# Kernel tuning notes

Measured on AMD Instinct MI355X. Metric: run time of the kernel, lower is better.

## Reference

```python
import jax, jax.numpy as jnp
import numpy as np

NUM_ITERATIONS = 100
EPS = 1e-6
LIPSCHITZ_COEFF = 0.9


def _l2_normalize(x, axis=None, eps=1e-12):
    return x * jax.lax.rsqrt((x * x).sum(axis=axis, keepdims=True) + eps)


def setup_inputs() -> dict:
    key = jax.random.key(0)
    k1, k2, k3, k4 = jax.random.split(key, 4)
    B, D_in, D_out = 32768, 1024, 1024
    x = jax.random.normal(k1, (B, D_in), dtype=jnp.float32)
    # TruncatedNormal(stddev=1/sqrt(fan_in)) approximated by scaled normal
    w = jax.random.normal(k2, (D_in, D_out), dtype=jnp.float32) / np.sqrt(D_in)
    b = jax.random.normal(k3, (D_out,), dtype=jnp.float32)
    u0 = jax.random.normal(k4, (1, D_out), dtype=jnp.float32)
    return {"x": x, "w": w, "b": b, "u0": u0}


def reference(x, w, b, u0):
    d_in = w.shape[0]

    # 100-step power iteration: tight sequential dependency chain of GEMV pairs.
    def body(i, carry):
        u, _ = carry
        v = _l2_normalize(jnp.matmul(u, w.T), eps=EPS)   # [1, d_in]
        u = _l2_normalize(jnp.matmul(v, w), eps=EPS)     # [1, d_out]
        return (u, v)

    v_init = jnp.zeros((1, d_in), dtype=w.dtype)
    u, v = jax.lax.fori_loop(0, NUM_ITERATIONS, body, (u0, v_init))
    u = jax.lax.stop_gradient(u)
    v = jax.lax.stop_gradient(v)

    sigma = jnp.matmul(jnp.matmul(v, w), u.T)[0, 0]      # spectral norm estimate
    factor = jnp.maximum(1.0, sigma / LIPSCHITZ_COEFF)
    w_norm = w / factor

    out = jnp.dot(x, w_norm) + b
    return out
```

## Files before the change

kernel.cpp:

```cpp
#include <hip/hip_runtime.h>
#include <hip/hip_bf16.h>
#include <cstdint>
#include <cstddef>

#define DDIM 1024
#define BROWS 32768

typedef __attribute__((ext_vector_type(8))) short short8;
typedef __attribute__((ext_vector_type(4))) float floatx4;

__device__ __forceinline__ float bf2f(unsigned short u) {
  return __uint_as_float(((unsigned int)u) << 16);
}
__device__ __forceinline__ unsigned short f2bf(float f) {
  unsigned int u = __float_as_uint(f);
  u += 0x7FFFu + ((u >> 16) & 1u);
  return (unsigned short)(u >> 16);
}

__device__ __forceinline__ void load_lds16(const void* g, void* l) {
  __builtin_amdgcn_global_load_lds(
      (const __attribute__((address_space(1))) unsigned int*)g,
      (__attribute__((address_space(3))) unsigned int*)l,
      16, 0, 0);
}

__global__ void __launch_bounds__(512, 2)
big_gemm(const float* __restrict__ Af, const unsigned short* __restrict__ Bt,
         float* __restrict__ Outf, const float* __restrict__ inv_ptr,
         const float* __restrict__ bias)
{
  __shared__ unsigned short As[128 * 32];
  __shared__ unsigned short Bs[256 * 32];

  const int tid  = threadIdx.x;
  const int lane = tid & 63;
  const int wid  = tid >> 6;
  const int wr = wid >> 2, wc = wid & 3;
  const int g = lane >> 4, r = lane & 15;

  const int bm0 = (int)(blockIdx.x & 255) * 128;
  const int bn0 = (int)(blockIdx.x >> 8) * 256;

  const floatx4 zero4 = {0.f, 0.f, 0.f, 0.f};
  floatx4 acc[4][4];
#pragma unroll
  for (int m = 0; m < 4; ++m)
#pragma unroll
    for (int n = 0; n < 4; ++n) acc[m][n] = zero4;

  for (int kk = 0; kk < DDIM; kk += 32) {
    __syncthreads();
#pragma unroll
    for (int p = 0; p < 2; ++p) {
      const int o = p * 8192 + tid * 16;
      const int row = o >> 6;
      const int cole = (o & 63) >> 1;
      load_lds16(Bt + (size_t)(bn0 + row) * DDIM + kk + cole, (char*)Bs + o);
    }
    {
      const int o = tid * 16;
      const int row = o >> 6;
      const int cole = (o & 63) >> 1;
      const float4* s = (const float4*)(Af + (size_t)(bm0 + row) * DDIM + kk + cole);
      float4 x0 = s[0], x1 = s[1];
      short8 t;
      t[0] = (short)f2bf(x0.x); t[1] = (short)f2bf(x0.y);
      t[2] = (short)f2bf(x0.z); t[3] = (short)f2bf(x0.w);
      t[4] = (short)f2bf(x1.x); t[5] = (short)f2bf(x1.y);
      t[6] = (short)f2bf(x1.z); t[7] = (short)f2bf(x1.w);
      *(short8*)((char*)As + o) = t;
    }
    __syncthreads();

    short8 afr[4], bfr[4];
#pragma unroll
    for (int m = 0; m < 4; ++m)
      afr[m] = *(const short8*)((const char*)As + (wr * 64 + m * 16 + r) * 64 + g * 16);
#pragma unroll
    for (int n = 0; n < 4; ++n)
      bfr[n] = *(const short8*)((const char*)Bs + (wc * 64 + n * 16 + r) * 64 + g * 16);
#pragma unroll
    for (int m = 0; m < 4; ++m)
#pragma unroll
      for (int n = 0; n < 4; ++n)
        acc[m][n] = __builtin_amdgcn_mfma_f32_16x16x32_bf16(afr[m], bfr[n], acc[m][n], 0, 0, 0);
  }

  const float inv = *inv_ptr;
#pragma unroll
  for (int n = 0; n < 4; ++n) {
    const int ocol = bn0 + wc * 64 + n * 16 + r;
    const float bv = bias[ocol];
#pragma unroll
    for (int m = 0; m < 4; ++m) {
      const int orow0 = bm0 + wr * 64 + m * 16 + g * 4;
#pragma unroll
      for (int q = 0; q < 4; ++q) {
        Outf[(size_t)(orow0 + q) * DDIM + ocol] = acc[m][n][q] * inv + bv;
      }
    }
  }
}

__global__ void __launch_bounds__(256, 2)
sq_gemm(const unsigned short* __restrict__ A, const unsigned short* __restrict__ Bt,
        unsigned short* __restrict__ Out, const float* __restrict__ in_max,
        float* __restrict__ out_max)
{
  __shared__ __align__(16) unsigned short As[2][4096];
  __shared__ __align__(16) unsigned short Bs[2][4096];
  __shared__ float redw[4];

  const int tid  = threadIdx.x;
  const int lane = tid & 63;
  const int wid  = tid >> 6;
  const int wr = wid >> 1, wc = wid & 1;
  const int g = lane >> 4, r = lane & 15;

  const int bm0 = (int)(blockIdx.x >> 4) * 64;
  const int bn0 = (int)(blockIdx.x & 15) * 64;

  const int so    = tid * 16;
  const int srow0 = so >> 7;
  const int sc16  = (so >> 4) & 7;
  const int scs   = sc16 ^ (srow0 & 7);
  const unsigned short* aSrc0 = A  + (size_t)(bm0 + srow0) * DDIM + scs * 8;
  const unsigned short* aSrc1 = A  + (size_t)(bm0 + 32 + srow0) * DDIM + scs * 8;
  const unsigned short* bSrc0 = Bt + (size_t)(bn0 + srow0) * DDIM + scs * 8;
  const unsigned short* bSrc1 = Bt + (size_t)(bn0 + 32 + srow0) * DDIM + scs * 8;

  const floatx4 zero4 = {0.f, 0.f, 0.f, 0.f};
  floatx4 acc[2][2];
#pragma unroll
  for (int fm = 0; fm < 2; ++fm)
#pragma unroll
    for (int fn = 0; fn < 2; ++fn) acc[fm][fn] = zero4;

  load_lds16(aSrc0, (char*)&As[0][0] + so);
  load_lds16(aSrc1, (char*)&As[0][0] + 4096 + so);
  load_lds16(bSrc0, (char*)&Bs[0][0] + so);
  load_lds16(bSrc1, (char*)&Bs[0][0] + 4096 + so);
  __syncthreads();

  int buf = 0;
  for (int t = 0; t < 16; ++t) {
    if (t + 1 < 16) {
      const int kk = (t + 1) * 64;
      load_lds16(aSrc0 + kk, (char*)&As[buf ^ 1][0] + so);
      load_lds16(aSrc1 + kk, (char*)&As[buf ^ 1][0] + 4096 + so);
      load_lds16(bSrc0 + kk, (char*)&Bs[buf ^ 1][0] + so);
      load_lds16(bSrc1 + kk, (char*)&Bs[buf ^ 1][0] + 4096 + so);
    }
#pragma unroll
    for (int ks = 0; ks < 2; ++ks) {
      const int chunk = ((ks << 2) + g) ^ (r & 7);
      short8 af[2], bf[2];
#pragma unroll
      for (int fm = 0; fm < 2; ++fm) {
        const int arow = wr * 32 + fm * 16 + r;
        af[fm] = *(const short8*)((const char*)&As[buf][0] + (arow << 7) + (chunk << 4));
      }
#pragma unroll
      for (int fn = 0; fn < 2; ++fn) {
        const int brow = wc * 32 + fn * 16 + r;
        bf[fn] = *(const short8*)((const char*)&Bs[buf][0] + (brow << 7) + (chunk << 4));
      }
#pragma unroll
      for (int fm = 0; fm < 2; ++fm)
#pragma unroll
        for (int fn = 0; fn < 2; ++fn)
          acc[fm][fn] = __builtin_amdgcn_mfma_f32_16x16x32_bf16(af[fm], bf[fn], acc[fm][fn], 0, 0, 0);
    }
    __syncthreads();
    buf ^= 1;
  }

  float c = 1.0f;
  if (in_max != nullptr) {
    int e;
    (void)frexpf(*in_max, &e);
    c = ldexpf(1.0f, -e);
  }
  const float c2 = c * c;
  float lmax = 0.0f;
#pragma unroll
  for (int fm = 0; fm < 2; ++fm) {
#pragma unroll
    for (int fn = 0; fn < 2; ++fn) {
      const int ocol = bn0 + wc * 32 + fn * 16 + r;
#pragma unroll
      for (int q = 0; q < 4; ++q) {
        const int orow = bm0 + wr * 32 + fm * 16 + g * 4 + q;
        float v = acc[fm][fn][q] * c2;
        Out[(size_t)orow * DDIM + ocol] = f2bf(v);
        lmax = fmaxf(lmax, fabsf(v));
      }
    }
  }
#pragma unroll
  for (int off = 32; off > 0; off >>= 1) lmax = fmaxf(lmax, __shfl_down(lmax, off));
  if (lane == 0) redw[wid] = lmax;
  __syncthreads();
  if (tid == 0) {
    float m = fmaxf(fmaxf(redw[0], redw[1]), fmaxf(redw[2], redw[3]));
    atomicMax((unsigned int*)out_max, __float_as_uint(m));
  }
}

__global__ void __launch_bounds__(256)
transpose_bf16(const float* __restrict__ W, unsigned short* __restrict__ WT)
{
  __shared__ float tile[64][65];
  const int bx = blockIdx.x & 15;
  const int by = blockIdx.x >> 4;
  const int tid = threadIdx.x;
  const int c = tid & 63;
  const int r0 = tid >> 6;
#pragma unroll
  for (int p = 0; p < 16; ++p) {
    int kr = p * 4 + r0;
    tile[kr][c] = W[(size_t)(bx * 64 + kr) * DDIM + by * 64 + c];
  }
  __syncthreads();
#pragma unroll
  for (int p = 0; p < 16; ++p) {
    int nr = p * 4 + r0;
    WT[(size_t)(by * 64 + nr) * DDIM + bx * 64 + c] = f2bf(tile[c][nr]);
  }
}

__global__ void __launch_bounds__(256)
gemv_pow(const unsigned short* __restrict__ P, const float* __restrict__ vin,
         float* __restrict__ vout)
{
  const int tid = threadIdx.x;
  const int lane = tid & 63;
  const int wid = tid >> 6;
  float vs[16];
  const float4* vv = (const float4*)(vin + lane * 16);
#pragma unroll
  for (int i = 0; i < 4; ++i) {
    float4 t = vv[i];
    vs[i * 4 + 0] = t.x; vs[i * 4 + 1] = t.y; vs[i * 4 + 2] = t.z; vs[i * 4 + 3] = t.w;
  }
#pragma unroll
  for (int rr = 0; rr < 4; ++rr) {
    const int row = (int)blockIdx.x * 16 + wid * 4 + rr;
    const unsigned short* pr = P + (size_t)row * DDIM + lane * 16;
    short8 p0 = *(const short8*)pr;
    short8 p1 = *(const short8*)(pr + 8);
    float s = 0.f;
#pragma unroll
    for (int e = 0; e < 8; ++e) s += bf2f((unsigned short)p0[e]) * vs[e];
#pragma unroll
    for (int e = 0; e < 8; ++e) s += bf2f((unsigned short)p1[e]) * vs[8 + e];
#pragma unroll
    for (int off = 32; off > 0; off >>= 1) s += __shfl_down(s, off);
    if (lane == 0) vout[row] = s * 0x1p-12f;
  }
}

__global__ void __launch_bounds__(256)
v_kernel(const float* __restrict__ W, const float* __restrict__ d,
         float* __restrict__ v_un, float* __restrict__ vpart)
{
  __shared__ float wsum[4];
  const int tid = threadIdx.x;
  const int lane = tid & 63;
  const int wid = tid >> 6;
  float vs[16];
  const float4* dv = (const float4*)(d + lane * 16);
#pragma unroll
  for (int i = 0; i < 4; ++i) {
    float4 t = dv[i];
    vs[i * 4 + 0] = t.x; vs[i * 4 + 1] = t.y; vs[i * 4 + 2] = t.z; vs[i * 4 + 3] = t.w;
  }
  float ssq = 0.f;
#pragma unroll
  for (int rr = 0; rr < 4; ++rr) {
    const int row = (int)blockIdx.x * 16 + wid * 4 + rr;
    const float4* wrow = (const float4*)(W + (size_t)row * DDIM + lane * 16);
    float s = 0.f;
#pragma unroll
    for (int i = 0; i < 4; ++i) {
      float4 t = wrow[i];
      s += t.x * vs[i * 4 + 0] + t.y * vs[i * 4 + 1] + t.z * vs[i * 4 + 2] + t.w * vs[i * 4 + 3];
    }
#pragma unroll
    for (int off = 32; off > 0; off >>= 1) s += __shfl_down(s, off);
    if (lane == 0) { v_un[row] = s; ssq += s * s; }
  }
  if (lane == 0) wsum[wid] = ssq;
  __syncthreads();
  if (tid == 0) vpart[blockIdx.x] = (wsum[0] + wsum[1]) + (wsum[2] + wsum[3]);
}

__global__ void __launch_bounds__(256)
t_fin_kernel(const float* __restrict__ W, const float* __restrict__ v_un,
             float* __restrict__ vpart, float* __restrict__ tpart,
             unsigned int* __restrict__ counter, float* __restrict__ inv_out)
{
  __shared__ float part[8][33];
  __shared__ unsigned int sticket;
  const int tid = threadIdx.x;
  const int col = (int)blockIdx.x * 32 + (tid & 31);
  const int ch = tid >> 5;
  float s = 0.f;
  const int i0 = ch * 128;
  for (int i = i0; i < i0 + 128; ++i)
    s += v_un[i] * W[(size_t)i * DDIM + col];
  part[ch][tid & 31] = s;
  __syncthreads();
  if (tid < 32) {
    float t = 0.f;
#pragma unroll
    for (int c2 = 0; c2 < 8; ++c2) t += part[c2][tid];
    part[0][tid] = t * t;
  }
  __syncthreads();
  if (tid == 0) {
    float ss = 0.f;
#pragma unroll
    for (int c = 0; c < 32; ++c) ss += part[0][c];
    tpart[blockIdx.x] = ss;
    __threadfence();
    sticket = atomicAdd(counter, 1u);
  }
  __syncthreads();
  if (sticket == 31) {
    __threadfence();
    float val = 0.f;
    if (tid < 64)
      val = __uint_as_float(atomicOr((unsigned int*)&vpart[tid], 0u));
    part[tid >> 5][tid & 31] = val;
    __syncthreads();
    if (tid == 0) {
      float sv = 0.f;
      for (int i = 0; i < 64; ++i) sv += part[i >> 5][i & 31];
      float stq = 0.f;
      for (int i = 0; i < 32; ++i)
        stq += __uint_as_float(atomicOr((unsigned int*)&tpart[i], 0u));
      float sigma = sqrtf(stq / sv);
      inv_out[0] = (sigma > 0.9f) ? (0.9f / sigma) : 1.0f;
    }
  }
}

extern "C" void kernel_launch(void* const* d_in, const int* in_sizes, int n_in,
                              void* d_out, int out_size, void* d_ws, size_t ws_size,
                              hipStream_t stream)
{
  const float* x  = (const float*)d_in[0];
  const float* w  = (const float*)d_in[1];
  const float* b  = (const float*)d_in[2];
  const float* u0 = (const float*)d_in[3];
  float* out = (float*)d_out;

  char* ws = (char*)d_ws;
  float* scal = (float*)ws;
  float* u_a  = (float*)(ws + 0x1000);
  float* u_b  = (float*)(ws + 0x2000);
  float* v_un = (float*)(ws + 0x3000);
  unsigned short* WT = (unsigned short*)(ws + 0x4000);
  unsigned short* P0 = (unsigned short*)(ws + 0x204000);
  unsigned short* P1 = (unsigned short*)(ws + 0x404000);

  hipMemsetAsync(d_ws, 0, 4096, stream);
  hipLaunchKernelGGL(transpose_bf16, dim3(256), dim3(256), 0, stream, w, WT);

  hipLaunchKernelGGL(sq_gemm, dim3(256), dim3(256), 0, stream,
                     WT, WT, P0, (const float*)nullptr, &scal[0]);
  hipLaunchKernelGGL(sq_gemm, dim3(256), dim3(256), 0, stream,
                     P0, P0, P1, &scal[0], &scal[1]);
  hipLaunchKernelGGL(sq_gemm, dim3(256), dim3(256), 0, stream,
                     P1, P1, P0, &scal[1], &scal[2]);
  hipLaunchKernelGGL(sq_gemm, dim3(256), dim3(256), 0, stream,
                     P0, P0, P1, &scal[2], &scal[3]);
  hipLaunchKernelGGL(sq_gemm, dim3(256), dim3(256), 0, stream,
                     P1, P1, P0, &scal[3], &scal[4]);
  hipLaunchKernelGGL(sq_gemm, dim3(256), dim3(256), 0, stream,
                     P0, P0, P1, &scal[4], &scal[5]);

  hipLaunchKernelGGL(gemv_pow, dim3(64), dim3(256), 0, stream, P1, u0, u_a);
  hipLaunchKernelGGL(gemv_pow, dim3(64), dim3(256), 0, stream, P1, u_a, u_b);
  hipLaunchKernelGGL(gemv_pow, dim3(64), dim3(256), 0, stream, P1, u_b, u_a);

  hipLaunchKernelGGL(v_kernel, dim3(64), dim3(256), 0, stream, w, u_a, v_un, &scal[16]);
  hipLaunchKernelGGL(t_fin_kernel, dim3(32), dim3(256), 0, stream,
                     w, v_un, &scal[16], &scal[80],
                     (unsigned int*)&scal[120], &scal[8]);

  hipLaunchKernelGGL(big_gemm, dim3(1024), dim3(512), 0, stream,
                     x, WT, out, &scal[8], b);
}
```

Measured before the change: 226.8 us.

## Double-buffer LDS tiles in big GEMM to overlap loads with MFMA

The main GEMM kernel now keeps two LDS stages. It prefetches the next K-slice of B via global_load_lds and the next fp32 A slice into registers while MFMAs run on the current stage, then converts A to bf16 and stores it after the compute. This cuts the loop from two barriers per K step to one and hides global load latency behind compute. The cost is a larger LDS footprint (48KB per block), which may limit the occupancy target of 2 blocks per CU, plus extra registers for the prefetched A values.

New measurement: 225.2 us, median of 2. No clear change (-0.7%).

```diff
diff --git a/kernel.cpp b/kernel.cpp
--- a/kernel.cpp
+++ b/kernel.cpp
@@ -30,8 +30,7 @@
          float* __restrict__ Outf, const float* __restrict__ inv_ptr,
          const float* __restrict__ bias)
 {
-  __shared__ unsigned short As[128 * 32];
-  __shared__ unsigned short Bs[256 * 32];
+  __shared__ __align__(16) char smem[49152];
 
   const int tid  = threadIdx.x;
   const int lane = tid & 63;
@@ -49,42 +48,74 @@
 #pragma unroll
     for (int n = 0; n < 4; ++n) acc[m][n] = zero4;
 
-  for (int kk = 0; kk < DDIM; kk += 32) {
-    __syncthreads();
+  const int ao   = tid * 16;
+  const int arow = ao >> 6;
+  const int acol = (ao & 63) >> 1;
+  const float* aSrc = Af + (size_t)(bm0 + arow) * DDIM + acol;
+
+  {
 #pragma unroll
     for (int p = 0; p < 2; ++p) {
       const int o = p * 8192 + tid * 16;
       const int row = o >> 6;
       const int cole = (o & 63) >> 1;
-      load_lds16(Bt + (size_t)(bn0 + row) * DDIM + kk + cole, (char*)Bs + o);
-    }
-    {
-      const int o = tid * 16;
-      const int row = o >> 6;
-      const int cole = (o & 63) >> 1;
-      const float4* s = (const float4*)(Af + (size_t)(bm0 + row) * DDIM + kk + cole);
-      float4 x0 = s[0], x1 = s[1];
-      short8 t;
-      t[0] = (short)f2bf(x0.x); t[1] = (short)f2bf(x0.y);
-      t[2] = (short)f2bf(x0.z); t[3] = (short)f2bf(x0.w);
-      t[4] = (short)f2bf(x1.x); t[5] = (short)f2bf(x1.y);
-      t[6] = (short)f2bf(x1.z); t[7] = (short)f2bf(x1.w);
-      *(short8*)((char*)As + o) = t;
-    }
-    __syncthreads();
+      load_lds16(Bt + (size_t)(bn0 + row) * DDIM + cole, smem + 16384 + o);
+    }
+    float4 x0 = *(const float4*)aSrc;
+    float4 x1 = *(const float4*)(aSrc + 4);
+    short8 t;
+    t[0] = (short)f2bf(x0.x); t[1] = (short)f2bf(x0.y);
+    t[2] = (short)f2bf(x0.z); t[3] = (short)f2bf(x0.w);
+    t[4] = (short)f2bf(x1.x); t[5] = (short)f2bf(x1.y);
+    t[6] = (short)f2bf(x1.z); t[7] = (short)f2bf(x1.w);
+    *(short8*)(smem + ao) = t;
+  }
+  __syncthreads();
+
+  for (int t = 0; t < 32; ++t) {
+    const int co = t & 1;
+    char* curA = smem + co * 8192;
+    char* curB = smem + 16384 + co * 16384;
+    char* nxtA = smem + (co ^ 1) * 8192;
+    char* nxtB = smem + 16384 + (co ^ 1) * 16384;
+
+    float4 pa0, pa1;
+    const bool pref = (t < 31);
+    if (pref) {
+      const int ko = (t + 1) * 32;
+#pragma unroll
+      for (int p = 0; p < 2; ++p) {
+        const int o = p * 8192 + tid * 16;
+        const int row = o >> 6;
+        const int cole = (o & 63) >> 1;
+        load_lds16(Bt + (size_t)(bn0 + row) * DDIM + ko + cole, nxtB + o);
+      }
+      pa0 = *(const float4*)(aSrc + ko);
+      pa1 = *(const float4*)(aSrc + ko + 4);
+    }
 
     short8 afr[4], bfr[4];
 #pragma unroll
     for (int m = 0; m < 4; ++m)
-      afr[m] = *(const short8*)((const char*)As + (wr * 64 + m * 16 + r) * 64 + g * 16);
+      afr[m] = *(const short8*)(curA + (wr * 64 + m * 16 + r) * 64 + g * 16);
 #pragma unroll
     for (int n = 0; n < 4; ++n)
-      bfr[n] = *(const short8*)((const char*)Bs + (wc * 64 + n * 16 + r) * 64 + g * 16);
+      bfr[n] = *(const short8*)(curB + (wc * 64 + n * 16 + r) * 64 + g * 16);
 #pragma unroll
     for (int m = 0; m < 4; ++m)
 #pragma unroll
       for (int n = 0; n < 4; ++n)
         acc[m][n] = __builtin_amdgcn_mfma_f32_16x16x32_bf16(afr[m], bfr[n], acc[m][n], 0, 0, 0);
+
+    if (pref) {
+      short8 tt;
+      tt[0] = (short)f2bf(pa0.x); tt[1] = (short)f2bf(pa0.y);
+      tt[2] = (short)f2bf(pa0.z); tt[3] = (short)f2bf(pa0.w);
+      tt[4] = (short)f2bf(pa1.x); tt[5] = (short)f2bf(pa1.y);
+      tt[6] = (short)f2bf(pa1.z); tt[7] = (short)f2bf(pa1.w);
+      *(short8*)(nxtA + ao) = tt;
+    }
+    __syncthreads();
   }
 
   const float inv = *inv_ptr;
```
